# Performance work log

Hardware: AMD Instinct MI355X
Metric: run time of the kernel (lower is better)

The kernel has to match this reference:

```python
import jax, jax.numpy as jnp
import numpy as np

HEAD_DIM = 128
NUM_Q_HEAD = 16
NUM_KV_HEAD = 4
WINDOW = 1024
SOFTMAX_CAP = 30.0
SOFTMAX_TEMP = 1.0
CLIP_L, CLIP_R = -0.03, 1.03
SCALE = 1.0 / np.sqrt(HEAD_DIM).astype(np.float32)


def setup_inputs() -> dict:
    key = jax.random.key(0)
    k1, k2, k3 = jax.random.split(key, 3)
    B, S = 2, 2048
    q = jax.random.normal(k1, (B, S, NUM_Q_HEAD, HEAD_DIM), jnp.float32)
    k = jax.random.normal(k2, (B, S, NUM_KV_HEAD, HEAD_DIM), jnp.float32)
    v = jax.random.normal(k3, (B, S, NUM_KV_HEAD, HEAD_DIM), jnp.float32)
    return {"q": q, "k": k, "v": v}


def _sliding_window_attn(q, k, v):
    # q: [B,S,Hq,D]; k,v: [B,S,Hkv,D]  (BSHD layout)
    n_rep = NUM_Q_HEAD // NUM_KV_HEAD
    k = jnp.repeat(k, n_rep, axis=2)  # GQA repeat-interleave -> [B,S,Hq,D]
    v = jnp.repeat(v, n_rep, axis=2)
    # BSHD -> BHSD
    q = q.transpose(0, 2, 1, 3)
    k = k.transpose(0, 2, 1, 3)
    v = v.transpose(0, 2, 1, 3)

    P = jnp.einsum('bhqd,bhkd->bhqk', q, k)  # raw scores [B,H,S,S]

    S = q.shape[2]
    qi = jnp.arange(S)[:, None]
    kj = jnp.arange(S)[None, :]
    # causal + sliding window: allow q_idx - window <= k_idx <= q_idx
    allowed = (kj <= qi) & (kj >= qi - WINDOW)
    mask = jnp.where(allowed, 0.0, -jnp.inf).astype(P.dtype)  # [S,S]

    # softmax capping: cap * tanh(P * scale / temp) + mask
    P = SOFTMAX_CAP * jnp.tanh(P * (SCALE / SOFTMAX_TEMP)) + mask

    A = jax.nn.softmax(P, axis=-1)  # numerically stable (max-subtracted)
    # softmax clipping: clamp((r-l)*A + l, 0, 1); dropout rate is 0 -> identity
    A = jnp.clip((CLIP_R - CLIP_L) * A + CLIP_L, 0.0, 1.0)

    O = jnp.einsum('bhqk,bhkd->bhqd', A, v)
    return O.transpose(0, 2, 1, 3)  # back to BSHD


def reference(q, k, v):
    return _sliding_window_attn(q, k, v)
```

## Files before the change

### kernel.cpp

```cpp
#include <hip/hip_runtime.h>
#include <hip/hip_bf16.h>

typedef float f32x4 __attribute__((ext_vector_type(4)));
typedef _Float16 f16x8 __attribute__((ext_vector_type(8)));
typedef unsigned int u32;

#define SQ   2048
#define HQ   16
#define HKV  4
#define DH   128
#define WIN  1024
#define QT   64
#define KT   64
#define WROW 36

#define AS1 __attribute__((address_space(1)))
#define AS3 __attribute__((address_space(3)))

__device__ __forceinline__ void gload16(const void* g, void* l) {
  __builtin_amdgcn_global_load_lds((const AS1 u32*)g, (AS3 u32*)l, 16, 0, 0);
}

#define BARW(N) do { __builtin_amdgcn_sched_barrier(0);                        \
  asm volatile("s_waitcnt vmcnt(" #N ")\n\ts_barrier" ::: "memory");           \
  __builtin_amdgcn_sched_barrier(0); } while (0)
#define BARP() do { __builtin_amdgcn_sched_barrier(0);                         \
  asm volatile("s_barrier" ::: "memory");                                      \
  __builtin_amdgcn_sched_barrier(0); } while (0)

__device__ __forceinline__ float swa_e(float s) {
  float u = __builtin_amdgcn_exp2f(s * 0.2550341464f);
  return __builtin_amdgcn_exp2f(-86.5617025f * __builtin_amdgcn_rcpf(u + 1.0f));
}

__global__ __launch_bounds__(256)
void prep(const float* __restrict__ K, const float* __restrict__ V,
          _Float16* __restrict__ kf, _Float16* __restrict__ vt)
{
  const int t = blockIdx.x * 256 + threadIdx.x;
  const int NK = 2 * HKV * SQ * 16;
  if (t < NK) {
    const int p  = t & 15;
    const int s  = (t >> 4) & (SQ - 1);
    const int hk = (t >> 15) & 3;
    const int b  = t >> 17;
    const int c  = p ^ (s & 7);
    const float* src = K + (((size_t)b * SQ + s) * HKV + hk) * DH + c * 8;
    f32x4 x0 = *(const f32x4*)src;
    f32x4 x1 = *(const f32x4*)(src + 4);
    f16x8 o;
    #pragma unroll
    for (int j = 0; j < 4; ++j) { o[j] = (_Float16)x0[j]; o[4 + j] = (_Float16)x1[j]; }
    *(f16x8*)(kf + (((size_t)(b * HKV + hk)) * SQ + s) * DH + p * 8) = o;
  } else {
    const int u   = t - NK;
    const int p   = u & 3;
    const int d   = (u >> 2) & 127;
    const int t32 = (u >> 9) & 63;
    const int hk  = (u >> 15) & 3;
    const int b   = u >> 17;
    const int c   = p ^ ((d >> 1) & 3);
    f16x8 o;
    #pragma unroll
    for (int j = 0; j < 8; ++j) {
      const int s = t32 * 32 + c * 8 + j;
      o[j] = (_Float16)V[(((size_t)b * SQ + s) * HKV + hk) * DH + d];
    }
    *(f16x8*)(vt + ((((size_t)(b * HKV + hk)) * 64 + t32) * DH + d) * 32 + p * 8) = o;
  }
}

__global__ __launch_bounds__(256, 4)
void swa_fwd(const float* __restrict__ Q, float* __restrict__ O,
             const _Float16* __restrict__ kf, const _Float16* __restrict__ vt)
{
  __shared__ _Float16 lbuf[16384];
  __shared__ _Float16 lW[4][16 * WROW];

  const int tid  = threadIdx.x;
  const int lane = tid & 63;
  const int wv   = tid >> 6;
  const int lm   = lane & 15;
  const int lg   = lane >> 4;

  const int bid    = blockIdx.x;
  const int stream = bid & 7;
  const int b      = stream >> 2;
  const int hk     = stream & 3;
  const int j      = bid >> 3;
  const int c      = j & 31;
  const int slot   = j >> 5;
  const int i      = c >> 2;
  const int hs     = c & 3;
  const int qt     = (slot == 0) ? (31 - i) : (slot == 1) ? (16 + i)
                   : (slot == 2) ? (15 - i) : i;
  const int h      = hk * 4 + hs;
  const int q0     = qt * QT;

  const _Float16* kfb = kf + ((size_t)(b * HKV + hk)) * SQ * DH;
  const char*     vtb = (const char*)(vt + ((size_t)(b * HKV + hk)) * 64 * DH * 32);

  f16x8 qa[4];
  {
    const int qrow = q0 + wv * 16 + lm;
    const float* qp = Q + (((size_t)b * SQ + qrow) * HQ + h) * DH;
    #pragma unroll
    for (int kb = 0; kb < 4; ++kb) {
      const float* p = qp + kb * 32 + lg * 8;
      f32x4 x0 = *(const f32x4*)p;
      f32x4 x1 = *(const f32x4*)(p + 4);
      f16x8 a;
      #pragma unroll
      for (int jj = 0; jj < 4; ++jj) { a[jj] = (_Float16)x0[jj]; a[4 + jj] = (_Float16)x1[jj]; }
      qa[kb] = a;
    }
  }

  const int kmin = (q0 - WIN) > 0 ? (q0 - WIN) : 0;
  const int nt   = (q0 + QT - kmin) / KT;
  const int qr0  = q0 + wv * 16 + lg * 4;

  #define STAGE16K(dstb, src) do {                                           \
    _Pragma("unroll")                                                        \
    for (int r4 = 0; r4 < 4; ++r4)                                           \
      gload16((const char*)(src) + r4 * 4096 + wv * 1024 + lane * 16,        \
              (char*)lbuf + (dstb) + r4 * 4096 + wv * 1024);                 \
  } while (0)
  #define STAGE8K(dstb, src) do {                                            \
    _Pragma("unroll")                                                        \
    for (int r2 = 0; r2 < 2; ++r2)                                           \
      gload16((const char*)(src) + r2 * 4096 + wv * 1024 + lane * 16,        \
              (char*)lbuf + (dstb) + r2 * 4096 + wv * 1024);                 \
  } while (0)

  float zs[4] = {0.f, 0.f, 0.f, 0.f};
  {
    STAGE16K(0, kfb + (size_t)kmin * DH);
    if (nt > 1) {
      STAGE16K(16384, kfb + (size_t)(kmin + KT) * DH);
      BARW(4);
    } else {
      BARW(0);
    }
    for (int t = 0; t < nt; ++t) {
      const char* cur  = (const char*)lbuf + (t & 1) * 16384;
      const int  kbase = kmin + t * KT;
      const bool peel  = (t == 0 && q0 >= WIN) || (t == nt - 1);
      #pragma unroll
      for (int ks = 0; ks < 4; ++ks) {
        f32x4 acc = {0.f, 0.f, 0.f, 0.f};
        const int keyl = ks * 16 + lm;
        #pragma unroll
        for (int kb = 0; kb < 4; ++kb) {
          const int chunk = (kb * 4 + lg) ^ (keyl & 7);
          f16x8 bf = *(const f16x8*)(cur + keyl * 256 + chunk * 16);
          acc = __builtin_amdgcn_mfma_f32_16x16x32_f16(qa[kb], bf, acc, 0, 0, 0);
        }
        if (peel) {
          const int key = kbase + keyl;
          #pragma unroll
          for (int r = 0; r < 4; ++r) {
            const int qr = qr0 + r;
            const bool ok = (key <= qr) && (key >= qr - WIN);
            zs[r] += ok ? swa_e(acc[r]) : 0.f;
          }
        } else {
          #pragma unroll
          for (int r = 0; r < 4; ++r) zs[r] += swa_e(acc[r]);
        }
      }
      BARP();
      if (t + 2 < nt) {
        STAGE16K((t & 1) * 16384, kfb + (size_t)(kmin + (t + 2) * KT) * DH);
        BARW(4);
      } else {
        BARW(0);
      }
    }
  }

  float rz[4], sthr[4];
  #pragma unroll
  for (int r = 0; r < 4; ++r) {
    float z = zs[r];
    z += __shfl_xor(z, 1);
    z += __shfl_xor(z, 2);
    z += __shfl_xor(z, 4);
    z += __shfl_xor(z, 8);
    rz[r] = 1.06f / z;
    float lt = __log2f(0.0283018868f * z);
    float A  = -86.5617024f / lt - 1.0f;
    float sv = 3.9204912f * __log2f(A) - 0.05f;
    sv = (lt >= 0.f) ? 1e30f : sv;
    sv = (lt <= -86.5617f) ? -1e30f : sv;
    sthr[r] = sv;
  }

  f32x4 oacc[8];
  #pragma unroll
  for (int ii = 0; ii < 8; ++ii) oacc[ii] = (f32x4){0.f, 0.f, 0.f, 0.f};

  const int nt2 = (q0 + QT - kmin) >> 5;
  STAGE8K(0,     kfb + (size_t)kmin * DH);
  STAGE8K(16384, vtb + (size_t)(kmin >> 5) * 8192);
  if (nt2 > 1) {
    STAGE8K(8192,         kfb + (size_t)(kmin + 32) * DH);
    STAGE8K(16384 + 8192, vtb + (size_t)((kmin >> 5) + 1) * 8192);
    BARW(4);
  } else {
    BARW(0);
  }

  const int vpc = lg ^ ((lm >> 1) & 3);

  for (int t2 = 0; t2 < nt2; ++t2) {
    const char* curK = (const char*)lbuf + (t2 & 1) * 8192;
    const char* curV = (const char*)lbuf + 16384 + (t2 & 1) * 8192;
    const int  kbase = kmin + t2 * 32;
    const bool peel  = ((q0 >= WIN) && (t2 <= 1)) || (t2 >= nt2 - 2);

    #pragma unroll
    for (int ks = 0; ks < 2; ++ks) {
      f32x4 acc = {0.f, 0.f, 0.f, 0.f};
      const int keyl = ks * 16 + lm;
      #pragma unroll
      for (int kb = 0; kb < 4; ++kb) {
        const int chunk = (kb * 4 + lg) ^ (keyl & 7);
        f16x8 bf = *(const f16x8*)(curK + keyl * 256 + chunk * 16);
        acc = __builtin_amdgcn_mfma_f32_16x16x32_f16(qa[kb], bf, acc, 0, 0, 0);
      }
      const int key = kbase + keyl;
      #pragma unroll
      for (int r = 0; r < 4; ++r) {
        float w = 0.f;
        if (__any(acc[r] > sthr[r])) {
          float e = swa_e(acc[r]);
          w = fminf(fmaxf(fmaf(e, rz[r], -0.03f), 0.f), 1.f);
          if (peel) {
            const int qr = qr0 + r;
            const bool ok = (key <= qr) && (key >= qr - WIN);
            w = ok ? w : 0.f;
          }
        }
        lW[wv][(lg * 4 + r) * WROW + ks * 16 + lm] = (_Float16)w;
      }
    }
    const f16x8 af = *(const f16x8*)&lW[wv][lm * WROW + lg * 8];
    #pragma unroll
    for (int dt = 0; dt < 8; ++dt) {
      const int d = dt * 16 + lm;
      f16x8 bf = *(const f16x8*)(curV + d * 64 + vpc * 16);
      oacc[dt] = __builtin_amdgcn_mfma_f32_16x16x32_f16(af, bf, oacc[dt], 0, 0, 0);
    }
    BARP();
    if (t2 + 2 < nt2) {
      const int kn = kmin + (t2 + 2) * 32;
      STAGE8K((t2 & 1) * 8192,         kfb + (size_t)kn * DH);
      STAGE8K(16384 + (t2 & 1) * 8192, vtb + (size_t)(kn >> 5) * 8192);
      BARW(4);
    } else {
      BARW(0);
    }
  }

  #pragma unroll
  for (int r = 0; r < 4; ++r) {
    float* op = O + (((size_t)b * SQ + (qr0 + r)) * HQ + h) * DH;
    #pragma unroll
    for (int dt = 0; dt < 8; ++dt) op[dt * 16 + lm] = oacc[dt][r];
  }
  #undef STAGE16K
  #undef STAGE8K
}

extern "C" void kernel_launch(void* const* d_in, const int* in_sizes, int n_in,
                              void* d_out, int out_size, void* d_ws, size_t ws_size,
                              hipStream_t stream) {
  const float* q = (const float*)d_in[0];
  const float* k = (const float*)d_in[1];
  const float* v = (const float*)d_in[2];
  float* o = (float*)d_out;

  _Float16* kf = (_Float16*)d_ws;
  _Float16* vt = kf + (size_t)2 * HKV * SQ * DH;

  hipLaunchKernelGGL(prep, dim3(2048), dim3(256), 0, stream, k, v, kf, vt);
  hipLaunchKernelGGL(swa_fwd, dim3(1024), dim3(256), 0, stream, q, o, kf, vt);
}
```

Measured before the change: 85.86 us.

## Split softmax denominator pass into separate split-K kernel with atomic accumulation

Moves the first pass, which computes the softmax normalizer for each query row, out of the fused kernel into a dedicated kernel. That kernel splits long key ranges into segments across 1536 blocks and accumulates partial sums with atomicAdd into a zeroed workspace buffer. The PV kernel then reads the normalizer from global memory instead of recomputing it. This is meant to balance load across query tiles and raise occupancy for the score pass, at the cost of an extra launch, a second read of Q, and atomic traffic.

```diff
diff --git a/kernel.cpp b/kernel.cpp
--- a/kernel.cpp
+++ b/kernel.cpp
@@ -11,7 +11,6 @@
 #define DH   128
 #define WIN  1024
 #define QT   64
-#define KT   64
 #define WROW 36
 
 #define AS1 __attribute__((address_space(1)))
@@ -35,9 +34,11 @@
 
 __global__ __launch_bounds__(256)
 void prep(const float* __restrict__ K, const float* __restrict__ V,
-          _Float16* __restrict__ kf, _Float16* __restrict__ vt)
+          _Float16* __restrict__ kf, _Float16* __restrict__ vt,
+          float* __restrict__ zbuf)
 {
   const int t = blockIdx.x * 256 + threadIdx.x;
+  if (t < 65536) zbuf[t] = 0.f;
   const int NK = 2 * HKV * SQ * 16;
   if (t < NK) {
     const int p  = t & 15;
@@ -70,9 +71,133 @@
   }
 }
 
+__global__ __launch_bounds__(256, 6)
+void zker(const float* __restrict__ Q, const _Float16* __restrict__ kf,
+          float* __restrict__ zbuf)
+{
+  __shared__ _Float16 lK[2][32 * DH];
+
+  const int tid  = threadIdx.x;
+  const int lane = tid & 63;
+  const int wv   = tid >> 6;
+  const int lm   = lane & 15;
+  const int lg   = lane >> 4;
+
+  const int bid    = blockIdx.x;
+  const int stream = bid & 7;
+  const int b      = stream >> 2;
+  const int hk     = stream & 3;
+  int qt, hs, s0, s1;
+  if (bid < 1024) {
+    const int m    = bid >> 3;
+    hs             = m & 3;
+    const int rest = m >> 2;
+    qt             = 16 + (rest & 15);
+    const int seg  = rest >> 4;
+    s0 = seg * 17; s1 = s0 + 17;
+  } else {
+    const int u    = bid - 1024;
+    const int half = u >> 8;
+    const int m    = (u & 255) >> 3;
+    hs             = m & 3;
+    const int j2   = m >> 2;
+    qt             = half ? j2 : (15 - j2);
+    s0 = 0; s1 = 2 * qt + 2;
+  }
+  const int h  = hk * 4 + hs;
+  const int q0 = qt * QT;
+
+  const _Float16* kfb = kf + ((size_t)(b * HKV + hk)) * SQ * DH;
+
+  f16x8 qa[4];
+  {
+    const int qrow = q0 + wv * 16 + lm;
+    const float* qp = Q + (((size_t)b * SQ + qrow) * HQ + h) * DH;
+    #pragma unroll
+    for (int kb = 0; kb < 4; ++kb) {
+      const float* p = qp + kb * 32 + lg * 8;
+      f32x4 x0 = *(const f32x4*)p;
+      f32x4 x1 = *(const f32x4*)(p + 4);
+      f16x8 a;
+      #pragma unroll
+      for (int jj = 0; jj < 4; ++jj) { a[jj] = (_Float16)x0[jj]; a[4 + jj] = (_Float16)x1[jj]; }
+      qa[kb] = a;
+    }
+  }
+
+  const int kmin = (q0 - WIN) > 0 ? (q0 - WIN) : 0;
+  const int nt2  = (q0 + QT - kmin) >> 5;
+  const int qr0  = q0 + wv * 16 + lg * 4;
+
+  #define ZSTG(dstb, src) do {                                               \
+    _Pragma("unroll")                                                        \
+    for (int r2 = 0; r2 < 2; ++r2)                                           \
+      gload16((const char*)(src) + r2 * 4096 + wv * 1024 + lane * 16,        \
+              (char*)lK + (dstb) + r2 * 4096 + wv * 1024);                   \
+  } while (0)
+
+  float zs[4] = {0.f, 0.f, 0.f, 0.f};
+  ZSTG((s0 & 1) * 8192, kfb + (size_t)(kmin + s0 * 32) * DH);
+  if (s0 + 1 < s1) {
+    ZSTG(((s0 + 1) & 1) * 8192, kfb + (size_t)(kmin + (s0 + 1) * 32) * DH);
+    BARW(2);
+  } else {
+    BARW(0);
+  }
+
+  for (int t2 = s0; t2 < s1; ++t2) {
+    const char* cur  = (const char*)lK + (t2 & 1) * 8192;
+    const int  kbase = kmin + t2 * 32;
+    const bool peel  = ((q0 >= WIN) && (t2 <= 1)) || (t2 >= nt2 - 2);
+    #pragma unroll
+    for (int ks = 0; ks < 2; ++ks) {
+      f32x4 acc = {0.f, 0.f, 0.f, 0.f};
+      const int keyl = ks * 16 + lm;
+      #pragma unroll
+      for (int kb = 0; kb < 4; ++kb) {
+        const int chunk = (kb * 4 + lg) ^ (keyl & 7);
+        f16x8 bf = *(const f16x8*)(cur + keyl * 256 + chunk * 16);
+        acc = __builtin_amdgcn_mfma_f32_16x16x32_f16(qa[kb], bf, acc, 0, 0, 0);
+      }
+      if (peel) {
+        const int key = kbase + keyl;
+        #pragma unroll
+        for (int r = 0; r < 4; ++r) {
+          const int qr = qr0 + r;
+          const bool ok = (key <= qr) && (key >= qr - WIN);
+          zs[r] += ok ? swa_e(acc[r]) : 0.f;
+        }
+      } else {
+        #pragma unroll
+        for (int r = 0; r < 4; ++r) zs[r] += swa_e(acc[r]);
+      }
+    }
+    BARP();
+    if (t2 + 2 < s1) {
+      ZSTG((t2 & 1) * 8192, kfb + (size_t)(kmin + (t2 + 2) * 32) * DH);
+      BARW(2);
+    } else {
+      BARW(0);
+    }
+  }
+
+  float* zrow = zbuf + ((size_t)(b * HQ + h)) * SQ;
+  #pragma unroll
+  for (int r = 0; r < 4; ++r) {
+    float z = zs[r];
+    z += __shfl_xor(z, 1);
+    z += __shfl_xor(z, 2);
+    z += __shfl_xor(z, 4);
+    z += __shfl_xor(z, 8);
+    if (lm == 0) atomicAdd(&zrow[qr0 + r], z);
+  }
+  #undef ZSTG
+}
+
 __global__ __launch_bounds__(256, 4)
-void swa_fwd(const float* __restrict__ Q, float* __restrict__ O,
-             const _Float16* __restrict__ kf, const _Float16* __restrict__ vt)
+void pvker(const float* __restrict__ Q, float* __restrict__ O,
+           const _Float16* __restrict__ kf, const _Float16* __restrict__ vt,
+           const float* __restrict__ zbuf)
 {
   __shared__ _Float16 lbuf[16384];
   __shared__ _Float16 lW[4][16 * WROW];
@@ -117,15 +242,25 @@
   }
 
   const int kmin = (q0 - WIN) > 0 ? (q0 - WIN) : 0;
-  const int nt   = (q0 + QT - kmin) / KT;
+  const int nt2  = (q0 + QT - kmin) >> 5;
   const int qr0  = q0 + wv * 16 + lg * 4;
 
-  #define STAGE16K(dstb, src) do {                                           \
-    _Pragma("unroll")                                                        \
-    for (int r4 = 0; r4 < 4; ++r4)                                           \
-      gload16((const char*)(src) + r4 * 4096 + wv * 1024 + lane * 16,        \
-              (char*)lbuf + (dstb) + r4 * 4096 + wv * 1024);                 \
-  } while (0)
+  float rz[4], sthr[4];
+  {
+    const float* zrow = zbuf + ((size_t)(b * HQ + h)) * SQ;
+    #pragma unroll
+    for (int r = 0; r < 4; ++r) {
+      const float z = zrow[qr0 + r];
+      rz[r] = 1.06f / z;
+      float lt = __log2f(0.0283018868f * z);
+      float A  = -86.5617024f / lt - 1.0f;
+      float sv = 3.9204912f * __log2f(A) - 0.05f;
+      sv = (lt >= 0.f) ? 1e30f : sv;
+      sv = (lt <= -86.5617f) ? -1e30f : sv;
+      sthr[r] = sv;
+    }
+  }
+
   #define STAGE8K(dstb, src) do {                                            \
     _Pragma("unroll")                                                        \
     for (int r2 = 0; r2 < 2; ++r2)                                           \
@@ -133,74 +268,10 @@
               (char*)lbuf + (dstb) + r2 * 4096 + wv * 1024);                 \
   } while (0)
 
-  float zs[4] = {0.f, 0.f, 0.f, 0.f};
-  {
-    STAGE16K(0, kfb + (size_t)kmin * DH);
-    if (nt > 1) {
-      STAGE16K(16384, kfb + (size_t)(kmin + KT) * DH);
-      BARW(4);
-    } else {
-      BARW(0);
-    }
-    for (int t = 0; t < nt; ++t) {
-      const char* cur  = (const char*)lbuf + (t & 1) * 16384;
-      const int  kbase = kmin + t * KT;
-      const bool peel  = (t == 0 && q0 >= WIN) || (t == nt - 1);
-      #pragma unroll
-      for (int ks = 0; ks < 4; ++ks) {
-        f32x4 acc = {0.f, 0.f, 0.f, 0.f};
-        const int keyl = ks * 16 + lm;
-        #pragma unroll
-        for (int kb = 0; kb < 4; ++kb) {
-          const int chunk = (kb * 4 + lg) ^ (keyl & 7);
-          f16x8 bf = *(const f16x8*)(cur + keyl * 256 + chunk * 16);
-          acc = __builtin_amdgcn_mfma_f32_16x16x32_f16(qa[kb], bf, acc, 0, 0, 0);
-        }
-        if (peel) {
-          const int key = kbase + keyl;
-          #pragma unroll
-          for (int r = 0; r < 4; ++r) {
-            const int qr = qr0 + r;
-            const bool ok = (key <= qr) && (key >= qr - WIN);
-            zs[r] += ok ? swa_e(acc[r]) : 0.f;
-          }
-        } else {
-          #pragma unroll
-          for (int r = 0; r < 4; ++r) zs[r] += swa_e(acc[r]);
-        }
-      }
-      BARP();
-      if (t + 2 < nt) {
-        STAGE16K((t & 1) * 16384, kfb + (size_t)(kmin + (t + 2) * KT) * DH);
-        BARW(4);
-      } else {
-        BARW(0);
-      }
-    }
-  }
-
-  float rz[4], sthr[4];
-  #pragma unroll
-  for (int r = 0; r < 4; ++r) {
-    float z = zs[r];
-    z += __shfl_xor(z, 1);
-    z += __shfl_xor(z, 2);
-    z += __shfl_xor(z, 4);
-    z += __shfl_xor(z, 8);
-    rz[r] = 1.06f / z;
-    float lt = __log2f(0.0283018868f * z);
-    float A  = -86.5617024f / lt - 1.0f;
-    float sv = 3.9204912f * __log2f(A) - 0.05f;
-    sv = (lt >= 0.f) ? 1e30f : sv;
-    sv = (lt <= -86.5617f) ? -1e30f : sv;
-    sthr[r] = sv;
-  }
-
   f32x4 oacc[8];
   #pragma unroll
   for (int ii = 0; ii < 8; ++ii) oacc[ii] = (f32x4){0.f, 0.f, 0.f, 0.f};
 
-  const int nt2 = (q0 + QT - kmin) >> 5;
   STAGE8K(0,     kfb + (size_t)kmin * DH);
   STAGE8K(16384, vtb + (size_t)(kmin >> 5) * 8192);
   if (nt2 > 1) {
@@ -269,7 +340,6 @@
     #pragma unroll
     for (int dt = 0; dt < 8; ++dt) op[dt * 16 + lm] = oacc[dt][r];
   }
-  #undef STAGE16K
   #undef STAGE8K
 }
 
@@ -281,9 +351,11 @@
   const float* v = (const float*)d_in[2];
   float* o = (float*)d_out;
 
-  _Float16* kf = (_Float16*)d_ws;
-  _Float16* vt = kf + (size_t)2 * HKV * SQ * DH;
-
-  hipLaunchKernelGGL(prep, dim3(2048), dim3(256), 0, stream, k, v, kf, vt);
-  hipLaunchKernelGGL(swa_fwd, dim3(1024), dim3(256), 0, stream, q, o, kf, vt);
-}
+  _Float16* kf   = (_Float16*)d_ws;
+  _Float16* vt   = kf + (size_t)2 * HKV * SQ * DH;
+  float*    zbuf = (float*)((char*)d_ws + 8388608);
+
+  hipLaunchKernelGGL(prep,  dim3(2048), dim3(256), 0, stream, k, v, kf, vt, zbuf);
+  hipLaunchKernelGGL(zker,  dim3(1536), dim3(256), 0, stream, q, kf, zbuf);
+  hipLaunchKernelGGL(pvker, dim3(1024), dim3(256), 0, stream, q, o, kf, vt, zbuf);
+}
```

Result: slower. 95.21 us (+10.9%).
